# Performance work log

Hardware: AMD Instinct MI355X
Metric: run time of the kernel (lower is better)

## Reference

```python
import jax, jax.numpy as jnp
import numpy as np

# SparseSphereConv (graph_level=6 -> V=40962, kernel_size=9, stride=1, select_index=None)
# Pipeline: neighbor gather -> data-dependent nonzero row selection ->
# per-vertex KxK interpolation matmul -> 1xK conv (linear over C_in,K) -> scatter back.
# With stride=1 / select_index=None the static selection is the identity, so the
# dynamic nonzero selection is equivalent to computing all rows and zeroing the
# rows whose gathered features are entirely zero (selected rows are scattered back,
# unselected rows stay 0 in sparse_reset's zero-initialized output).

BS, C_IN, C_OUT, V, K = 4, 32, 32, 40962, 9

def setup_inputs() -> dict:
    key = jax.random.key(0)
    k1, k2, k3, k4, k5 = jax.random.split(key, 5)
    x = jax.random.normal(k1, (BS, C_IN, V), dtype=jnp.float32)
    index = jax.random.randint(k2, (V, K), 0, V, dtype=jnp.int32)          # neighbor ids per vertex
    itp_mat = jax.random.uniform(k3, (V, K, K), dtype=jnp.float32)         # per-vertex interpolation
    conv_w = jax.random.normal(k4, (C_OUT, C_IN, K), dtype=jnp.float32) * 0.05  # Conv2d(C_in,C_out,(1,K)) weight
    conv_b = jax.random.normal(k5, (C_OUT,), dtype=jnp.float32) * 0.05
    return {"x": x, "index": index, "itp_mat": itp_mat, "conv_w": conv_w, "conv_b": conv_b}

def reference(x, index, itp_mat, conv_w, conv_b):
    # x: [bs, C, V] -> permute(2,0,1) -> gather neighbors -> [V, K, bs, C]
    g = jnp.transpose(x, (2, 0, 1))[index]
    g = jnp.transpose(g, (3, 2, 0, 1))                      # [C, bs, V, K]  (== reshape of [C, bs*V, K])
    # sparse_prepare: keep rows whose min or max over (C, K) is nonzero (detached in torch)
    gd = jax.lax.stop_gradient(g)
    rmin = gd.min(axis=(0, 3))                              # [bs, V]
    rmax = gd.max(axis=(0, 3))                              # [bs, V]
    mask = (rmin != 0) | (rmax != 0)                        # [bs, V]
    # Interploate: [C, S, 1, K] @ [S, K, K] per row -> batched small matmul
    interp = jnp.einsum('cbvk,vkj->cbvj', g, itp_mat)       # [C, bs, V, K]
    # Conv2d with kernel (1, K): contraction over (C_in, K) + bias
    out = jnp.einsum('cbvk,ock->bov', interp, conv_w) + conv_b[None, :, None]  # [bs, C_out, V]
    # sparse_reset: rows not selected stay zero
    return out * mask[:, None, :].astype(out.dtype)
```

## Files before the change

### kernel.cpp

```cpp
#include <hip/hip_runtime.h>
#include <hip/hip_bf16.h>

#define NV 40962
#define NK 9
#define CIN 32
#define COUT 32
#define NBS 4
#define VT 256
#define TP 260
#define NT 2561
#define NV81 (NV * 81)
#define NV9  (NV * 9)

typedef __attribute__((ext_vector_type(8))) short bf16x8;
typedef __attribute__((ext_vector_type(4))) float f32x4;
typedef __attribute__((ext_vector_type(2))) float f32x2;

#define PKFMA_L(A, G, R) asm("v_pk_fma_f32 %0, %1, %2, %0 op_sel:[0,0,0] op_sel_hi:[0,1,1]" : "+v"(A) : "v"(G), "v"(R))
#define PKFMA_H(A, G, R) asm("v_pk_fma_f32 %0, %1, %2, %0 op_sel:[1,0,0] op_sel_hi:[1,1,1]" : "+v"(A) : "v"(G), "v"(R))
#define PKMUL_L(A, G, R) asm("v_pk_mul_f32 %0, %1, %2 op_sel:[0,0] op_sel_hi:[0,1]" : "=v"(A) : "v"(G), "v"(R))
#define PKMUL_H(A, G, R) asm("v_pk_mul_f32 %0, %1, %2 op_sel:[1,0] op_sel_hi:[1,1]" : "=v"(A) : "v"(G), "v"(R))

#define ACC(cc, j) ((j) == 8 ? acc8[cc] : (((j) & 1) ? acc2[cc][(j) >> 1].y \
                                                     : acc2[cc][(j) >> 1].x))

__device__ __forceinline__ unsigned pkbf(float a, float b) {
    union { __hip_bfloat162 h2; unsigned u; } cv;
    cv.h2 = __float22bfloat162_rn(make_float2(a, b));
    return cv.u;
}

__global__ void __launch_bounds__(256) transpose_x_bf16(
    const float* __restrict__ x, unsigned* __restrict__ xtw)
{
    __shared__ unsigned T[16 * TP];
    const int b  = blockIdx.x & 3;
    const int v0 = (blockIdx.x >> 2) * VT;
    const int t  = threadIdx.x;
    const int w  = t >> 6;
    const int L  = t & 63;
    const bool full = (v0 + VT <= NV);

    #pragma unroll
    for (int i = 0; i < 4; ++i) {
        const int q = w + 4 * i;
        const float* rowA = x + (size_t)(b * 32 + 2 * q) * NV;
        const float* rowB = rowA + NV;
        #pragma unroll
        for (int h = 0; h < 2; ++h) {
            const int vl = 128 * h + 2 * L;
            float2 a, c;
            if (full) {
                a = *(const float2*)(rowA + v0 + vl);
                c = *(const float2*)(rowB + v0 + vl);
            } else {
                const int v = v0 + vl;
                a.x = (v     < NV) ? rowA[v]     : 0.0f;
                a.y = (v + 1 < NV) ? rowA[v + 1] : 0.0f;
                c.x = (v     < NV) ? rowB[v]     : 0.0f;
                c.y = (v + 1 < NV) ? rowB[v + 1] : 0.0f;
            }
            uint2 d;
            d.x = pkbf(a.x, c.x);
            d.y = pkbf(a.y, c.y);
            *(uint2*)&T[q * TP + vl] = d;
        }
    }
    __syncthreads();

    #pragma unroll
    for (int i = 0; i < 4; ++i) {
        const int vl = i * 64 + w * 16 + (L >> 2);
        const int u4 = L & 3;
        const int v  = v0 + vl;
        if (v < NV) {
            uint4 d;
            d.x = T[(4 * u4 + 0) * TP + vl];
            d.y = T[(4 * u4 + 1) * TP + vl];
            d.z = T[(4 * u4 + 2) * TP + vl];
            d.w = T[(4 * u4 + 3) * TP + vl];
            *(uint4*)&xtw[(size_t)v * 64 + u4 * 16 + b * 4] = d;
        }
    }
}

__global__ void __launch_bounds__(256) convert_w_bf16(
    const float* __restrict__ w, unsigned short* __restrict__ wbf)
{
    const int i = blockIdx.x * 256 + threadIdx.x;
    if (i < COUT * CIN * NK) {
        const int o = i / 288;
        const int r = i - o * 288;
        const int c = r / 9;
        const int j = r - c * 9;
        unsigned u = __float_as_uint(w[i]);
        wbf[o * 288 + j * 32 + c] =
            (unsigned short)((u + 0x7FFFu + ((u >> 16) & 1u)) >> 16);
    }
}

__global__ void __launch_bounds__(256) sparse_conv_mfma(
    const unsigned short* __restrict__ xt, const int* __restrict__ index,
    const float* __restrict__ itp, const unsigned short* __restrict__ wbf,
    const float* __restrict__ bias, float* __restrict__ out)
{
    __shared__ unsigned short Wlds[9 * 32 * 32];
    __shared__ float itp_s[16 * 108];
    __shared__ int   idx_s[144];

    const int t    = threadIdx.x;
    const int w    = t >> 6;
    const int lane = t & 63;
    const int arow = lane & 15;
    const int coct = lane >> 4;
    const int b    = (lane >> 2) & 3;
    const int vv   = lane & 3;
    const int vl   = w * 4 + vv;
    const int tile = blockIdx.x;

    float bs0[4], bs1[4];
    #pragma unroll
    for (int r = 0; r < 4; ++r) {
        bs0[r] = bias[coct * 4 + r];
        bs1[r] = bias[coct * 4 + 16 + r];
    }

    #pragma unroll
    for (int r = 0; r < 5; ++r) {
        const int n = t + r * 256;
        if (n < 1152) {
            const int j  = n >> 7;
            const int o  = (n >> 2) & 31;
            const int cq = n & 3;
            ((uint4*)Wlds)[n] = ((const uint4*)wbf)[o * 36 + j * 4 + cq];
        }
    }
    if (t < 144) {
        const size_t bix = (size_t)tile * 144 + t;
        idx_s[t] = (bix < (size_t)NV9) ? index[bix] : 0;
    }
    {
        float itpv[6];
        const size_t base = (size_t)tile * 1296;
        #pragma unroll
        for (int i = 0; i < 6; ++i) {
            const int o = i * 256 + t;
            itpv[i] = (o < 1296 && base + o < (size_t)NV81) ? itp[base + o]
                                                            : 0.0f;
        }
        #pragma unroll
        for (int i = 0; i < 6; ++i) {
            const int o = i * 256 + t;
            if (o < 1296) {
                const int vli = o / 81;
                const int r2 = o - vli * 81;
                const int kk = r2 / 9;
                const int jj = r2 - kk * 9;
                itp_s[vli * 108 + kk * 12 + jj] = itpv[i];
            }
        }
    }
    __syncthreads();

    int nbr[NK];
    #pragma unroll
    for (int n = 0; n < NK; ++n) nbr[n] = idx_s[vl * 9 + n];

    const unsigned short* gbase = xt + coct * 32 + b * 8;
    uint4 g[NK];
    #pragma unroll
    for (int n = 0; n < NK; ++n)
        g[n] = *(const uint4*)(gbase + (size_t)nbr[n] * 128);

    unsigned frag[9][4];
    unsigned nzbits = 0;
    const float* ib = &itp_s[vl * 108];

    #pragma unroll
    for (int h = 0; h < 2; ++h) {
        f32x2 acc2[4][4];
        float acc8[4];
        #pragma unroll
        for (int n = 0; n < NK; ++n) {
            const uint2 gk = h ? make_uint2(g[n].z, g[n].w)
                               : make_uint2(g[n].x, g[n].y);
            nzbits |= (gk.x | gk.y) & 0x7FFF7FFFu;
            f32x2 gp01, gp23;
            gp01.x = __uint_as_float(gk.x << 16);
            gp01.y = __uint_as_float(gk.x & 0xFFFF0000u);
            gp23.x = __uint_as_float(gk.y << 16);
            gp23.y = __uint_as_float(gk.y & 0xFFFF0000u);
            const float* ir = ib + n * 12;
            const f32x4 ra = *(const f32x4*)ir;
            const f32x4 rb = *(const f32x4*)(ir + 4);
            const float r8 = ir[8];
            f32x2 rp[4];
            rp[0] = __builtin_shufflevector(ra, ra, 0, 1);
            rp[1] = __builtin_shufflevector(ra, ra, 2, 3);
            rp[2] = __builtin_shufflevector(rb, rb, 0, 1);
            rp[3] = __builtin_shufflevector(rb, rb, 2, 3);
            if (n == 0) {
                #pragma unroll
                for (int jp = 0; jp < 4; ++jp) {
                    PKMUL_L(acc2[0][jp], gp01, rp[jp]);
                    PKMUL_H(acc2[1][jp], gp01, rp[jp]);
                    PKMUL_L(acc2[2][jp], gp23, rp[jp]);
                    PKMUL_H(acc2[3][jp], gp23, rp[jp]);
                }
                acc8[0] = gp01.x * r8; acc8[1] = gp01.y * r8;
                acc8[2] = gp23.x * r8; acc8[3] = gp23.y * r8;
            } else {
                #pragma unroll
                for (int jp = 0; jp < 4; ++jp) {
                    PKFMA_L(acc2[0][jp], gp01, rp[jp]);
                    PKFMA_H(acc2[1][jp], gp01, rp[jp]);
                    PKFMA_L(acc2[2][jp], gp23, rp[jp]);
                    PKFMA_H(acc2[3][jp], gp23, rp[jp]);
                }
                acc8[0] += gp01.x * r8; acc8[1] += gp01.y * r8;
                acc8[2] += gp23.x * r8; acc8[3] += gp23.y * r8;
            }
        }
        #pragma unroll
        for (int ks = 0; ks < 9; ++ks) {
            frag[ks][2 * h]     = pkbf(ACC(0, ks), ACC(1, ks));
            frag[ks][2 * h + 1] = pkbf(ACC(2, ks), ACC(3, ks));
        }
    }

    unsigned nzw = nzbits;
    nzw |= __shfl_xor(nzw, 16);
    nzw |= __shfl_xor(nzw, 32);

    f32x4 c0 = {0.f, 0.f, 0.f, 0.f};
    f32x4 c1 = {0.f, 0.f, 0.f, 0.f};
    #pragma unroll
    for (int ks = 0; ks < 9; ++ks) {
        union { uint4 u; bf16x8 v; } bfr;
        bfr.u.x = frag[ks][0]; bfr.u.y = frag[ks][1];
        bfr.u.z = frag[ks][2]; bfr.u.w = frag[ks][3];
        const bf16x8 wa0 =
            *(const bf16x8*)&Wlds[(ks * 32 + arow) * 32 + coct * 8];
        const bf16x8 wa1 =
            *(const bf16x8*)&Wlds[(ks * 32 + arow + 16) * 32 + coct * 8];
        c0 = __builtin_amdgcn_mfma_f32_16x16x32_bf16(wa0, bfr.v, c0, 0, 0, 0);
        c1 = __builtin_amdgcn_mfma_f32_16x16x32_bf16(wa1, bfr.v, c1, 0, 0, 0);
    }

    const int vglob = tile * 16 + vl;
    if (vglob < NV) {
        const float m = nzw ? 1.0f : 0.0f;
        float* ob = out + (size_t)b * (COUT * NV) + vglob;
        #pragma unroll
        for (int r = 0; r < 4; ++r) {
            ob[(size_t)(coct * 4 + r) * NV]      = (c0[r] + bs0[r]) * m;
            ob[(size_t)(coct * 4 + 16 + r) * NV] = (c1[r] + bs1[r]) * m;
        }
    }
}

extern "C" void kernel_launch(void* const* d_in, const int* in_sizes, int n_in,
                              void* d_out, int out_size, void* d_ws, size_t ws_size,
                              hipStream_t stream)
{
    const float* x     = (const float*)d_in[0];
    const int*   index = (const int*)  d_in[1];
    const float* itp   = (const float*)d_in[2];
    const float* w     = (const float*)d_in[3];
    const float* bias  = (const float*)d_in[4];
    float*       out   = (float*)d_out;

    unsigned short* xt  = (unsigned short*)d_ws;
    unsigned short* wbf = (unsigned short*)((char*)d_ws + (size_t)NV * 256);

    hipLaunchKernelGGL(convert_w_bf16, dim3((COUT * CIN * NK + 255) / 256),
                       dim3(256), 0, stream, w, wbf);
    const int vtiles = (NV + VT - 1) / VT;
    hipLaunchKernelGGL(transpose_x_bf16, dim3(vtiles * NBS), dim3(256), 0,
                       stream, x, (unsigned*)xt);
    hipLaunchKernelGGL(sparse_conv_mfma, dim3(NT), dim3(256), 0,
                       stream, xt, index, itp, wbf, bias, out);
}
```

Measured before the change: 135.9 us.

## Process two vertex tiles per block to amortize weight staging and overlap gathers

Each block now handles two 16-vertex tiles instead of one, halving the grid. The weight LDS staging and bias loads are shared across both tiles. Both tiles' itp and index data are staged up front, and both sets of neighbour gathers are issued before any compute, so more loads are in flight. The nonzero check is hoisted out of the interpolation loop. The cost is higher register pressure from holding 18 uint4 gathers, which may lower occupancy, and a smaller grid with less parallelism.

```diff
diff --git a/kernel.cpp b/kernel.cpp
--- a/kernel.cpp
+++ b/kernel.cpp
@@ -9,6 +9,7 @@
 #define VT 256
 #define TP 260
 #define NT 2561
+#define NB 1281
 #define NV81 (NV * 81)
 #define NV9  (NV * 9)
 
@@ -99,82 +100,19 @@
     }
 }
 
-__global__ void __launch_bounds__(256) sparse_conv_mfma(
-    const unsigned short* __restrict__ xt, const int* __restrict__ index,
-    const float* __restrict__ itp, const unsigned short* __restrict__ wbf,
-    const float* __restrict__ bias, float* __restrict__ out)
-{
-    __shared__ unsigned short Wlds[9 * 32 * 32];
-    __shared__ float itp_s[16 * 108];
-    __shared__ int   idx_s[144];
-
-    const int t    = threadIdx.x;
-    const int w    = t >> 6;
-    const int lane = t & 63;
-    const int arow = lane & 15;
-    const int coct = lane >> 4;
-    const int b    = (lane >> 2) & 3;
-    const int vv   = lane & 3;
-    const int vl   = w * 4 + vv;
-    const int tile = blockIdx.x;
-
-    float bs0[4], bs1[4];
-    #pragma unroll
-    for (int r = 0; r < 4; ++r) {
-        bs0[r] = bias[coct * 4 + r];
-        bs1[r] = bias[coct * 4 + 16 + r];
-    }
-
-    #pragma unroll
-    for (int r = 0; r < 5; ++r) {
-        const int n = t + r * 256;
-        if (n < 1152) {
-            const int j  = n >> 7;
-            const int o  = (n >> 2) & 31;
-            const int cq = n & 3;
-            ((uint4*)Wlds)[n] = ((const uint4*)wbf)[o * 36 + j * 4 + cq];
-        }
-    }
-    if (t < 144) {
-        const size_t bix = (size_t)tile * 144 + t;
-        idx_s[t] = (bix < (size_t)NV9) ? index[bix] : 0;
-    }
-    {
-        float itpv[6];
-        const size_t base = (size_t)tile * 1296;
-        #pragma unroll
-        for (int i = 0; i < 6; ++i) {
-            const int o = i * 256 + t;
-            itpv[i] = (o < 1296 && base + o < (size_t)NV81) ? itp[base + o]
-                                                            : 0.0f;
-        }
-        #pragma unroll
-        for (int i = 0; i < 6; ++i) {
-            const int o = i * 256 + t;
-            if (o < 1296) {
-                const int vli = o / 81;
-                const int r2 = o - vli * 81;
-                const int kk = r2 / 9;
-                const int jj = r2 - kk * 9;
-                itp_s[vli * 108 + kk * 12 + jj] = itpv[i];
-            }
-        }
-    }
-    __syncthreads();
-
-    int nbr[NK];
-    #pragma unroll
-    for (int n = 0; n < NK; ++n) nbr[n] = idx_s[vl * 9 + n];
-
-    const unsigned short* gbase = xt + coct * 32 + b * 8;
-    uint4 g[NK];
+__device__ __forceinline__ void tile_compute(
+    const uint4* g, const float* __restrict__ ib,
+    const unsigned short* __restrict__ Wlds,
+    const float* bs0, const float* bs1, float* __restrict__ out,
+    int tile, int vl, int arow, int coct, int b)
+{
+    unsigned frag[9][4];
+
+    unsigned nzbits = 0;
     #pragma unroll
     for (int n = 0; n < NK; ++n)
-        g[n] = *(const uint4*)(gbase + (size_t)nbr[n] * 128);
-
-    unsigned frag[9][4];
-    unsigned nzbits = 0;
-    const float* ib = &itp_s[vl * 108];
+        nzbits |= (g[n].x | g[n].y | g[n].z | g[n].w);
+    nzbits &= 0x7FFF7FFFu;
 
     #pragma unroll
     for (int h = 0; h < 2; ++h) {
@@ -184,7 +122,6 @@
         for (int n = 0; n < NK; ++n) {
             const uint2 gk = h ? make_uint2(g[n].z, g[n].w)
                                : make_uint2(g[n].x, g[n].y);
-            nzbits |= (gk.x | gk.y) & 0x7FFF7FFFu;
             f32x2 gp01, gp23;
             gp01.x = __uint_as_float(gk.x << 16);
             gp01.y = __uint_as_float(gk.x & 0xFFFF0000u);
@@ -259,6 +196,98 @@
     }
 }
 
+__global__ void __launch_bounds__(256) sparse_conv_mfma(
+    const unsigned short* __restrict__ xt, const int* __restrict__ index,
+    const float* __restrict__ itp, const unsigned short* __restrict__ wbf,
+    const float* __restrict__ bias, float* __restrict__ out)
+{
+    __shared__ unsigned short Wlds[9 * 32 * 32];
+    __shared__ float itp_s[2][16 * 108];
+    __shared__ int   idx_s[2][144];
+
+    const int t    = threadIdx.x;
+    const int w    = t >> 6;
+    const int lane = t & 63;
+    const int arow = lane & 15;
+    const int coct = lane >> 4;
+    const int b    = (lane >> 2) & 3;
+    const int vv   = lane & 3;
+    const int vl   = w * 4 + vv;
+    const int t0   = blockIdx.x * 2;
+
+    float bs0[4], bs1[4];
+    #pragma unroll
+    for (int r = 0; r < 4; ++r) {
+        bs0[r] = bias[coct * 4 + r];
+        bs1[r] = bias[coct * 4 + 16 + r];
+    }
+
+    #pragma unroll
+    for (int r = 0; r < 5; ++r) {
+        const int n = t + r * 256;
+        if (n < 1152) {
+            const int j  = n >> 7;
+            const int o  = (n >> 2) & 31;
+            const int cq = n & 3;
+            ((uint4*)Wlds)[n] = ((const uint4*)wbf)[o * 36 + j * 4 + cq];
+        }
+    }
+    #pragma unroll
+    for (int tt = 0; tt < 2; ++tt) {
+        if (t < 144) {
+            const size_t bix = (size_t)(t0 + tt) * 144 + t;
+            idx_s[tt][t] = (bix < (size_t)NV9) ? index[bix] : 0;
+        }
+    }
+    {
+        float va[6], vb[6];
+        const size_t baseA = (size_t)t0 * 1296;
+        const size_t baseB = baseA + 1296;
+        #pragma unroll
+        for (int i = 0; i < 6; ++i) {
+            const int o = i * 256 + t;
+            va[i] = (o < 1296 && baseA + o < (size_t)NV81) ? itp[baseA + o]
+                                                           : 0.0f;
+            vb[i] = (o < 1296 && baseB + o < (size_t)NV81) ? itp[baseB + o]
+                                                           : 0.0f;
+        }
+        #pragma unroll
+        for (int i = 0; i < 6; ++i) {
+            const int o = i * 256 + t;
+            if (o < 1296) {
+                const int vli = o / 81;
+                const int r2  = o - vli * 81;
+                const int kk  = r2 / 9;
+                const int jj  = r2 - kk * 9;
+                const int off = vli * 108 + kk * 12 + jj;
+                itp_s[0][off] = va[i];
+                itp_s[1][off] = vb[i];
+            }
+        }
+    }
+    __syncthreads();
+
+    int nbrA[NK], nbrB[NK];
+    #pragma unroll
+    for (int n = 0; n < NK; ++n) nbrA[n] = idx_s[0][vl * 9 + n];
+    #pragma unroll
+    for (int n = 0; n < NK; ++n) nbrB[n] = idx_s[1][vl * 9 + n];
+
+    const unsigned short* gbase = xt + coct * 32 + b * 8;
+    uint4 gA[NK], gB[NK];
+    #pragma unroll
+    for (int n = 0; n < NK; ++n)
+        gA[n] = *(const uint4*)(gbase + (size_t)nbrA[n] * 128);
+    #pragma unroll
+    for (int n = 0; n < NK; ++n)
+        gB[n] = *(const uint4*)(gbase + (size_t)nbrB[n] * 128);
+
+    tile_compute(gA, &itp_s[0][vl * 108], Wlds, bs0, bs1, out,
+                 t0, vl, arow, coct, b);
+    tile_compute(gB, &itp_s[1][vl * 108], Wlds, bs0, bs1, out,
+                 t0 + 1, vl, arow, coct, b);
+}
+
 extern "C" void kernel_launch(void* const* d_in, const int* in_sizes, int n_in,
                               void* d_out, int out_size, void* d_ws, size_t ws_size,
                               hipStream_t stream)
@@ -278,6 +307,6 @@
     const int vtiles = (NV + VT - 1) / VT;
     hipLaunchKernelGGL(transpose_x_bf16, dim3(vtiles * NBS), dim3(256), 0,
                        stream, x, (unsigned*)xt);
-    hipLaunchKernelGGL(sparse_conv_mfma, dim3(NT), dim3(256), 0,
+    hipLaunchKernelGGL(sparse_conv_mfma, dim3(NB), dim3(256), 0,
                        stream, xt, index, itp, wbf, bias, out);
 }
```

Measured after the change: 128.3 us. 5.6% less time.

## Fuse weight conversion into transpose and drop block-level LDS staging in conv

Applied to the files above, without the earlier changes.

The weight bf16 conversion moves into the transpose kernel, saving one launch, and the transpose now handles 64-vertex chunks across all batches. In the main kernel the shared weight tile and block-wide __syncthreads are removed. Each lane loads its MFMA weight fragments straight from global memory into registers, neighbour indices are spread with wave shuffles, and itp is staged per wave behind only a wave barrier. This cuts LDS use and block sync, at the cost of many more registers per thread (18 uint4 weight fragments) and redundant global weight loads.

```diff
diff --git a/kernel.cpp b/kernel.cpp
--- a/kernel.cpp
+++ b/kernel.cpp
@@ -5,9 +5,6 @@
 #define NK 9
 #define CIN 32
 #define COUT 32
-#define NBS 4
-#define VT 256
-#define TP 260
 #define NT 2561
 #define NV81 (NV * 81)
 #define NV9  (NV * 9)
@@ -31,82 +28,72 @@
 }
 
 __global__ void __launch_bounds__(256) transpose_x_bf16(
-    const float* __restrict__ x, unsigned* __restrict__ xtw)
-{
-    __shared__ unsigned T[16 * TP];
-    const int b  = blockIdx.x & 3;
-    const int v0 = (blockIdx.x >> 2) * VT;
-    const int t  = threadIdx.x;
-    const int w  = t >> 6;
-    const int L  = t & 63;
-    const bool full = (v0 + VT <= NV);
-
-    #pragma unroll
-    for (int i = 0; i < 4; ++i) {
-        const int q = w + 4 * i;
-        const float* rowA = x + (size_t)(b * 32 + 2 * q) * NV;
-        const float* rowB = rowA + NV;
-        #pragma unroll
-        for (int h = 0; h < 2; ++h) {
-            const int vl = 128 * h + 2 * L;
-            float2 a, c;
-            if (full) {
-                a = *(const float2*)(rowA + v0 + vl);
-                c = *(const float2*)(rowB + v0 + vl);
-            } else {
-                const int v = v0 + vl;
-                a.x = (v     < NV) ? rowA[v]     : 0.0f;
-                a.y = (v + 1 < NV) ? rowA[v + 1] : 0.0f;
-                c.x = (v     < NV) ? rowB[v]     : 0.0f;
-                c.y = (v + 1 < NV) ? rowB[v + 1] : 0.0f;
-            }
-            uint2 d;
-            d.x = pkbf(a.x, c.x);
-            d.y = pkbf(a.y, c.y);
-            *(uint2*)&T[q * TP + vl] = d;
-        }
-    }
-    __syncthreads();
-
-    #pragma unroll
-    for (int i = 0; i < 4; ++i) {
-        const int vl = i * 64 + w * 16 + (L >> 2);
-        const int u4 = L & 3;
-        const int v  = v0 + vl;
-        if (v < NV) {
-            uint4 d;
-            d.x = T[(4 * u4 + 0) * TP + vl];
-            d.y = T[(4 * u4 + 1) * TP + vl];
-            d.z = T[(4 * u4 + 2) * TP + vl];
-            d.w = T[(4 * u4 + 3) * TP + vl];
-            *(uint4*)&xtw[(size_t)v * 64 + u4 * 16 + b * 4] = d;
-        }
-    }
-}
-
-__global__ void __launch_bounds__(256) convert_w_bf16(
+    const float* __restrict__ x, unsigned* __restrict__ xtw,
     const float* __restrict__ w, unsigned short* __restrict__ wbf)
 {
-    const int i = blockIdx.x * 256 + threadIdx.x;
-    if (i < COUT * CIN * NK) {
-        const int o = i / 288;
-        const int r = i - o * 288;
+    __shared__ unsigned U[64 * 65];
+    const int t = threadIdx.x;
+
+    const int ci = blockIdx.x * 256 + t;
+    if (ci < COUT * CIN * NK) {
+        const int o = ci / 288;
+        const int r = ci - o * 288;
         const int c = r / 9;
         const int j = r - c * 9;
-        unsigned u = __float_as_uint(w[i]);
+        unsigned u = __float_as_uint(w[ci]);
         wbf[o * 288 + j * 32 + c] =
             (unsigned short)((u + 0x7FFFu + ((u >> 16) & 1u)) >> 16);
     }
-}
-
-__global__ void __launch_bounds__(256) sparse_conv_mfma(
+
+    const int v0  = blockIdx.x * 64;
+    const int l16 = t & 15;
+    const int p   = t >> 4;
+
+    #pragma unroll
+    for (int i = 0; i < 4; ++i) {
+        const int q    = p * 4 + i;
+        const int r0   = 2 * q;
+        const int bb   = r0 >> 5;
+        const int c0   = r0 & 31;
+        const int dwb  = (c0 >> 3) * 16 + bb * 4 + ((c0 & 7) >> 1);
+        const float* rowA = x + (size_t)r0 * NV + v0;
+        const float* rowB = rowA + NV;
+        #pragma unroll
+        for (int hv = 0; hv < 2; ++hv) {
+            const int v = l16 * 2 + hv * 32;
+            float2 a = make_float2(0.f, 0.f), c2 = make_float2(0.f, 0.f);
+            if (v0 + v < NV) {
+                a  = *(const float2*)(rowA + v);
+                c2 = *(const float2*)(rowB + v);
+            }
+            U[(v    ) * 65 + dwb] = pkbf(a.x, c2.x);
+            U[(v + 1) * 65 + dwb] = pkbf(a.y, c2.y);
+        }
+    }
+    __syncthreads();
+
+    const int v  = t >> 2;
+    const int qo = t & 3;
+    if (v0 + v < NV) {
+        #pragma unroll
+        for (int j = 0; j < 4; ++j) {
+            const int n = j * 4 + qo;
+            uint4 d;
+            d.x = U[v * 65 + n * 4 + 0];
+            d.y = U[v * 65 + n * 4 + 1];
+            d.z = U[v * 65 + n * 4 + 2];
+            d.w = U[v * 65 + n * 4 + 3];
+            *(uint4*)&xtw[(size_t)(v0 + v) * 64 + n * 4] = d;
+        }
+    }
+}
+
+__global__ void __launch_bounds__(256, 2) sparse_conv_mfma(
     const unsigned short* __restrict__ xt, const int* __restrict__ index,
     const float* __restrict__ itp, const unsigned short* __restrict__ wbf,
     const float* __restrict__ bias, float* __restrict__ out)
 {
-    __shared__ unsigned short Wlds[9 * 32 * 32];
-    __shared__ float itp_s[16 * 108];
-    __shared__ int   idx_s[144];
+    __shared__ float itp_s[4][4][108];
 
     const int t    = threadIdx.x;
     const int w    = t >> 6;
@@ -115,8 +102,27 @@
     const int coct = lane >> 4;
     const int b    = (lane >> 2) & 3;
     const int vv   = lane & 3;
-    const int vl   = w * 4 + vv;
     const int tile = blockIdx.x;
+
+    int ia = tile * 144 + w * 36 + (lane < 36 ? lane : 35);
+    ia = ia < NV9 ? ia : NV9 - 1;
+    const int myidx = index[ia];
+
+    float iv[6];
+    const size_t ibase = (size_t)(tile * 16 + w * 4) * 81;
+    #pragma unroll
+    for (int i = 0; i < 6; ++i) {
+        const int o = i * 64 + lane;
+        iv[i] = (o < 324 && ibase + o < (size_t)NV81) ? itp[ibase + o] : 0.0f;
+    }
+
+    const unsigned short* wb0 = wbf + arow * 288 + coct * 8;
+    uint4 wa0[NK], wa1[NK];
+    #pragma unroll
+    for (int ks = 0; ks < NK; ++ks) {
+        wa0[ks] = *(const uint4*)(wb0 + ks * 32);
+        wa1[ks] = *(const uint4*)(wb0 + 16 * 288 + ks * 32);
+    }
 
     float bs0[4], bs1[4];
     #pragma unroll
@@ -125,57 +131,36 @@
         bs1[r] = bias[coct * 4 + 16 + r];
     }
 
-    #pragma unroll
-    for (int r = 0; r < 5; ++r) {
-        const int n = t + r * 256;
-        if (n < 1152) {
-            const int j  = n >> 7;
-            const int o  = (n >> 2) & 31;
-            const int cq = n & 3;
-            ((uint4*)Wlds)[n] = ((const uint4*)wbf)[o * 36 + j * 4 + cq];
-        }
-    }
-    if (t < 144) {
-        const size_t bix = (size_t)tile * 144 + t;
-        idx_s[t] = (bix < (size_t)NV9) ? index[bix] : 0;
-    }
-    {
-        float itpv[6];
-        const size_t base = (size_t)tile * 1296;
-        #pragma unroll
-        for (int i = 0; i < 6; ++i) {
-            const int o = i * 256 + t;
-            itpv[i] = (o < 1296 && base + o < (size_t)NV81) ? itp[base + o]
-                                                            : 0.0f;
-        }
-        #pragma unroll
-        for (int i = 0; i < 6; ++i) {
-            const int o = i * 256 + t;
-            if (o < 1296) {
-                const int vli = o / 81;
-                const int r2 = o - vli * 81;
-                const int kk = r2 / 9;
-                const int jj = r2 - kk * 9;
-                itp_s[vli * 108 + kk * 12 + jj] = itpv[i];
-            }
-        }
-    }
-    __syncthreads();
-
     int nbr[NK];
     #pragma unroll
-    for (int n = 0; n < NK; ++n) nbr[n] = idx_s[vl * 9 + n];
-
+    for (int n = 0; n < NK; ++n) nbr[n] = __shfl(myidx, vv * 9 + n);
     const unsigned short* gbase = xt + coct * 32 + b * 8;
     uint4 g[NK];
     #pragma unroll
     for (int n = 0; n < NK; ++n)
         g[n] = *(const uint4*)(gbase + (size_t)nbr[n] * 128);
 
+    #pragma unroll
+    for (int i = 0; i < 6; ++i) {
+        const int o = i * 64 + lane;
+        if (o < 324) {
+            const int vloc = o / 81;
+            const int r2   = o - vloc * 81;
+            const int kk   = r2 / 9;
+            const int jj   = r2 - kk * 9;
+            itp_s[w][vloc][kk * 12 + jj] = iv[i];
+        }
+    }
+    __builtin_amdgcn_wave_barrier();
+
     unsigned frag[9][4];
     unsigned nzbits = 0;
-    const float* ib = &itp_s[vl * 108];
-
+    #pragma unroll
+    for (int n = 0; n < NK; ++n)
+        nzbits |= (g[n].x | g[n].y | g[n].z | g[n].w);
+    nzbits &= 0x7FFF7FFFu;
+
+    const float* ib = &itp_s[w][vv][0];
     #pragma unroll
     for (int h = 0; h < 2; ++h) {
         f32x2 acc2[4][4];
@@ -184,7 +169,6 @@
         for (int n = 0; n < NK; ++n) {
             const uint2 gk = h ? make_uint2(g[n].z, g[n].w)
                                : make_uint2(g[n].x, g[n].y);
-            nzbits |= (gk.x | gk.y) & 0x7FFF7FFFu;
             f32x2 gp01, gp23;
             gp01.x = __uint_as_float(gk.x << 16);
             gp01.y = __uint_as_float(gk.x & 0xFFFF0000u);
@@ -236,18 +220,16 @@
     f32x4 c1 = {0.f, 0.f, 0.f, 0.f};
     #pragma unroll
     for (int ks = 0; ks < 9; ++ks) {
-        union { uint4 u; bf16x8 v; } bfr;
+        union { uint4 u; bf16x8 v; } bfr, au0, au1;
         bfr.u.x = frag[ks][0]; bfr.u.y = frag[ks][1];
         bfr.u.z = frag[ks][2]; bfr.u.w = frag[ks][3];
-        const bf16x8 wa0 =
-            *(const bf16x8*)&Wlds[(ks * 32 + arow) * 32 + coct * 8];
-        const bf16x8 wa1 =
-            *(const bf16x8*)&Wlds[(ks * 32 + arow + 16) * 32 + coct * 8];
-        c0 = __builtin_amdgcn_mfma_f32_16x16x32_bf16(wa0, bfr.v, c0, 0, 0, 0);
-        c1 = __builtin_amdgcn_mfma_f32_16x16x32_bf16(wa1, bfr.v, c1, 0, 0, 0);
-    }
-
-    const int vglob = tile * 16 + vl;
+        au0.u = wa0[ks];
+        au1.u = wa1[ks];
+        c0 = __builtin_amdgcn_mfma_f32_16x16x32_bf16(au0.v, bfr.v, c0, 0, 0, 0);
+        c1 = __builtin_amdgcn_mfma_f32_16x16x32_bf16(au1.v, bfr.v, c1, 0, 0, 0);
+    }
+
+    const int vglob = tile * 16 + w * 4 + vv;
     if (vglob < NV) {
         const float m = nzw ? 1.0f : 0.0f;
         float* ob = out + (size_t)b * (COUT * NV) + vglob;
@@ -273,11 +255,9 @@
     unsigned short* xt  = (unsigned short*)d_ws;
     unsigned short* wbf = (unsigned short*)((char*)d_ws + (size_t)NV * 256);
 
-    hipLaunchKernelGGL(convert_w_bf16, dim3((COUT * CIN * NK + 255) / 256),
-                       dim3(256), 0, stream, w, wbf);
-    const int vtiles = (NV + VT - 1) / VT;
-    hipLaunchKernelGGL(transpose_x_bf16, dim3(vtiles * NBS), dim3(256), 0,
-                       stream, x, (unsigned*)xt);
+    const int vchunks = (NV + 63) / 64;
+    hipLaunchKernelGGL(transpose_x_bf16, dim3(vchunks), dim3(256), 0,
+                       stream, x, (unsigned*)xt, w, wbf);
     hipLaunchKernelGGL(sparse_conv_mfma, dim3(NT), dim3(256), 0,
                        stream, xt, index, itp, wbf, bias, out);
 }
```

Result: faster. 124.2 us (-8.6%).
